# Performance work log

Hardware: AMD Instinct MI355X
Metric: run time of the kernel (lower is better)

The kernel has to match this reference:

```python
import jax, jax.numpy as jnp
import numpy as np

B, K, D, H, ZDIM = 65536, 16, 64, 128, 16

def setup_inputs() -> dict:
    key = jax.random.key(0)
    ks = jax.random.split(key, 20)
    s = 0.05
    inp = {
        'z': jax.random.normal(ks[0], (B, ZDIM), dtype=jnp.float32),
        'y': jax.random.randint(ks[1], (B,), 0, K),
        # backbone: 4 fc blocks (Linear+ReLU)
        'bw0': jax.random.normal(ks[2], (ZDIM, H), dtype=jnp.float32) * s,
        'bb0': jnp.zeros((H,), dtype=jnp.float32),
        'bw1': jax.random.normal(ks[3], (H, H), dtype=jnp.float32) * s,
        'bb1': jnp.zeros((H,), dtype=jnp.float32),
        'bw2': jax.random.normal(ks[4], (H, H), dtype=jnp.float32) * s,
        'bb2': jnp.zeros((H,), dtype=jnp.float32),
        'bw3': jax.random.normal(ks[5], (H, H), dtype=jnp.float32) * s,
        'bb3': jnp.zeros((H,), dtype=jnp.float32),
        # K heads, weights stacked on leading expert axis; layers 0-2 have ReLU, layer 3 does not
        'hw0': jax.random.normal(ks[6], (K, H, H), dtype=jnp.float32) * s,
        'hb0': jnp.zeros((K, H), dtype=jnp.float32),
        'hw1': jax.random.normal(ks[7], (K, H, H), dtype=jnp.float32) * s,
        'hb1': jnp.zeros((K, H), dtype=jnp.float32),
        'hw2': jax.random.normal(ks[8], (K, H, H), dtype=jnp.float32) * s,
        'hb2': jnp.zeros((K, H), dtype=jnp.float32),
        'hw3': jax.random.normal(ks[9], (K, H, D), dtype=jnp.float32) * s,
        'hb3': jnp.zeros((K, D), dtype=jnp.float32),
    }
    return inp

def reference(z, y, bw0, bb0, bw1, bb1, bw2, bb2, bw3, bb3,
              hw0, hb0, hw1, hb1, hw2, hb2, hw3, hb3):
    h = jax.nn.relu(z @ bw0 + bb0)
    h = jax.nn.relu(h @ bw1 + bb1)
    h = jax.nn.relu(h @ bw2 + bb2)
    h = jax.nn.relu(h @ bw3 + bb3)          # [B, H]
    # all K expert heads (faithful to original: compute all, then gather)
    a = jax.nn.relu(jnp.einsum('bi,kij->bkj', h, hw0) + hb0)  # [B, K, H]
    a = jax.nn.relu(jnp.einsum('bki,kij->bkj', a, hw1) + hb1)
    a = jax.nn.relu(jnp.einsum('bki,kij->bkj', a, hw2) + hb2)
    a = jnp.einsum('bki,kij->bkj', a, hw3) + hb3              # [B, K, D], no ReLU
    # select the y-th head per sample
    out = jnp.take_along_axis(a, y[:, None, None], axis=1)[:, 0, :]  # [B, D]
    return out
```

## Files before the change

kernel.cpp:

```cpp
#include <hip/hip_runtime.h>
#include <hip/hip_bf16.h>
#include <stdint.h>


typedef _Float16 f16;
typedef __attribute__((ext_vector_type(4)))  _Float16 f16x4;
typedef __attribute__((ext_vector_type(8)))  _Float16 f16x8;
typedef __attribute__((ext_vector_type(16))) float    f32x16;
typedef uint32_t u32;

#define MFMA(a, b, c) __builtin_amdgcn_mfma_f32_32x32x16_f16((a), (b), (c), 0, 0, 0)

constexpr int Bc = 65536;
constexpr int Kc = 16;
constexpr int Hc = 128;
constexpr int Dc = 64;

constexpr int CAP  = 4608;
constexpr int BPE  = CAP / 64;
constexpr int NBLK = Kc * BPE;

constexpr float INV_LOSCALE = 1.0f / 1024.0f;

constexpr int BBW_F16 = 2048 + 3 * 16384;
constexpr int HWE_F16 = 3 * 16384 + 8192;

constexpr int PREP_BLKS = 52 + Kc * 56;

__device__ __forceinline__ f32x16 zero16() {
    f32x16 z;
#pragma unroll
    for (int i = 0; i < 16; ++i) z[i] = 0.0f;
    return z;
}

__device__ __forceinline__ int actOff(int s, int u) {
    return s * 128 + ((u ^ (s & 15)) << 3);
}

template<bool RELU>
__device__ __forceinline__ void epi_store(
    const f32x16& aH0, const f32x16& aL0,
    const f32x16& aH1, const f32x16& aL1,
    const float* biasLds, f16* aOut, int wid, int l31, int bh)
{
#pragma unroll
    for (int rg = 0; rg < 4; ++rg) {
        const float4 bv = *(const float4*)(biasLds + 32 * wid + 8 * rg + 4 * bh);
        const float bb[4] = {bv.x, bv.y, bv.z, bv.w};
#pragma unroll
        for (int mt = 0; mt < 2; ++mt) {
            const f32x16& aH = mt ? aH1 : aH0;
            const f32x16& aL = mt ? aL1 : aL0;
            f16x4 h4;
#pragma unroll
            for (int j = 0; j < 4; ++j) {
                float v = fmaf(aL[4 * rg + j], INV_LOSCALE, aH[4 * rg + j]) + bb[j];
                if (RELU) v = fmaxf(v, 0.0f);
                h4[j] = (f16)v;
            }
            const int s = 32 * mt + l31;
            *(f16x4*)(aOut + actOff(s, 4 * wid + rg) + 4 * bh) = h4;
        }
    }
}

__device__ __forceinline__ void layer4(
    const f16* __restrict__ Wh, const f16* __restrict__ Wl,
    const float* biasLds, const f16* aIn, f16* aOut,
    int wid, int lane, int l31, int bh)
{
    const f16* ph = Wh + wid * 4096 + lane * 8;
    const f16* pl = Wl + wid * 4096 + lane * 8;

    f32x16 aH0 = zero16(), aH1 = zero16(), aL0 = zero16(), aL1 = zero16();
#pragma unroll
    for (int ks = 0; ks < 8; ++ks) {
        const f16x8 whi = *(const f16x8*)(ph + ks * 512);
        const f16x8 wlo = *(const f16x8*)(pl + ks * 512);
        const f16x8 a0 = *(const f16x8*)(aIn + actOff(l31,      2 * ks + bh));
        const f16x8 a1 = *(const f16x8*)(aIn + actOff(32 + l31, 2 * ks + bh));
        aH0 = MFMA(whi, a0, aH0);
        aH1 = MFMA(whi, a1, aH1);
        aL0 = MFMA(wlo, a0, aL0);
        aL1 = MFMA(wlo, a1, aL1);
    }
    epi_store<true>(aH0, aL0, aH1, aL1, biasLds, aOut, wid, l31, bh);
}

__global__ __launch_bounds__(256, 3) void fused_mlp(
    const float* __restrict__ z,
    const int* __restrict__ idxb, const int* __restrict__ cursor,
    const f16* __restrict__ bbH, const f16* __restrict__ bbL,
    const float* __restrict__ bb0, const float* __restrict__ bb1,
    const float* __restrict__ bb2, const float* __restrict__ bb3,
    const f16* __restrict__ hH, const f16* __restrict__ hL,
    const float* __restrict__ hb0, const float* __restrict__ hb1,
    const float* __restrict__ hb2, const float* __restrict__ hb3,
    float* __restrict__ out)
{
    __shared__ __attribute__((aligned(16))) f16 A[64 * 128];
    __shared__ __attribute__((aligned(16))) f16 B[64 * 128];
    __shared__ __attribute__((aligned(16))) float BIAS[960];
    __shared__ int sidx[64];

    const int blk = blockIdx.x;
    const int e = blk / BPE;
    const int local0 = (blk % BPE) * 64;
    const int cnt = min(cursor[e * 16], CAP);
    const int nvalid = cnt - local0;
    if (nvalid <= 0) return;

    const int tid = threadIdx.x;
    const int wid = tid >> 6, lane = tid & 63;
    const int l31 = lane & 31, bh = lane >> 5;

#pragma unroll
    for (int r = 0; r < 4; ++r) {
        const int i = r * 256 + tid;
        if (i < 960) {
            float v;
            if      (i < 128) v = bb0[i];
            else if (i < 256) v = bb1[i - 128];
            else if (i < 384) v = bb2[i - 256];
            else if (i < 512) v = bb3[i - 384];
            else if (i < 640) v = hb0[e * Hc + i - 512];
            else if (i < 768) v = hb1[e * Hc + i - 640];
            else if (i < 896) v = hb2[e * Hc + i - 768];
            else              v = hb3[e * Dc + i - 896];
            BIAS[i] = v;
        }
    }
    if (tid < 64) sidx[tid] = (tid < nvalid) ? idxb[e * CAP + local0 + tid] : -1;
    __syncthreads();

    {
        const int m = tid >> 2, q = tid & 3;
        const int b = sidx[m];
        f16x4 t;
        if (b >= 0) {
            const float4 v = *(const float4*)(z + (size_t)b * 16 + q * 4);
            t[0] = (f16)v.x; t[1] = (f16)v.y; t[2] = (f16)v.z; t[3] = (f16)v.w;
        } else {
            t[0] = t[1] = t[2] = t[3] = (f16)0.0f;
        }
        *(f16x4*)(A + actOff(m, q >> 1) + (q & 1) * 4) = t;
    }
    __syncthreads();

    {
        const f16x8 w0h = *(const f16x8*)(bbH + wid * 512 + lane * 8);
        const f16x8 w0l = *(const f16x8*)(bbL + wid * 512 + lane * 8);
        const f16x8 a0 = *(const f16x8*)(A + actOff(l31,      bh));
        const f16x8 a1 = *(const f16x8*)(A + actOff(32 + l31, bh));
        f32x16 aH0 = zero16(), aH1 = zero16(), aL0 = zero16(), aL1 = zero16();
        aH0 = MFMA(w0h, a0, aH0);
        aH1 = MFMA(w0h, a1, aH1);
        aL0 = MFMA(w0l, a0, aL0);
        aL1 = MFMA(w0l, a1, aL1);
        epi_store<true>(aH0, aL0, aH1, aL1, BIAS, B, wid, l31, bh);
    }
    __syncthreads();

    layer4(bbH + 2048,  bbL + 2048,  BIAS + 128, B, A, wid, lane, l31, bh);
    __syncthreads();
    layer4(bbH + 18432, bbL + 18432, BIAS + 256, A, B, wid, lane, l31, bh);
    __syncthreads();
    layer4(bbH + 34816, bbL + 34816, BIAS + 384, B, A, wid, lane, l31, bh);
    __syncthreads();

    const size_t we = (size_t)e * HWE_F16;
    layer4(hH + we,         hL + we,         BIAS + 512, A, B, wid, lane, l31, bh);
    __syncthreads();
    layer4(hH + we + 16384, hL + we + 16384, BIAS + 640, B, A, wid, lane, l31, bh);
    __syncthreads();
    layer4(hH + we + 32768, hL + we + 32768, BIAS + 768, A, B, wid, lane, l31, bh);
    __syncthreads();

    if (wid < 2) {
        const f16* ph = hH + we + 49152 + wid * 4096 + lane * 8;
        const f16* pl = hL + we + 49152 + wid * 4096 + lane * 8;
        f32x16 aH0 = zero16(), aH1 = zero16(), aL0 = zero16(), aL1 = zero16();
#pragma unroll
        for (int ks = 0; ks < 8; ++ks) {
            const f16x8 whi = *(const f16x8*)(ph + ks * 512);
            const f16x8 wlo = *(const f16x8*)(pl + ks * 512);
            const f16x8 a0 = *(const f16x8*)(B + actOff(l31,      2 * ks + bh));
            const f16x8 a1 = *(const f16x8*)(B + actOff(32 + l31, 2 * ks + bh));
            aH0 = MFMA(whi, a0, aH0);
            aH1 = MFMA(whi, a1, aH1);
            aL0 = MFMA(wlo, a0, aL0);
            aL1 = MFMA(wlo, a1, aL1);
        }
#pragma unroll
        for (int mt = 0; mt < 2; ++mt) {
            const int b = sidx[32 * mt + l31];
            if (b < 0) continue;
            const f32x16& aH = mt ? aH1 : aH0;
            const f32x16& aL = mt ? aL1 : aL0;
#pragma unroll
            for (int rg = 0; rg < 4; ++rg) {
                const int nb = 32 * wid + 8 * rg + 4 * bh;
                const float4 bv = *(const float4*)(BIAS + 896 + nb);
                float4 v;
                v.x = fmaf(aL[4 * rg + 0], INV_LOSCALE, aH[4 * rg + 0]) + bv.x;
                v.y = fmaf(aL[4 * rg + 1], INV_LOSCALE, aH[4 * rg + 1]) + bv.y;
                v.z = fmaf(aL[4 * rg + 2], INV_LOSCALE, aH[4 * rg + 2]) + bv.z;
                v.w = fmaf(aL[4 * rg + 3], INV_LOSCALE, aH[4 * rg + 3]) + bv.w;
                *(float4*)(out + (size_t)b * Dc + nb) = v;
            }
        }
    }
}

__global__ void prep_scatter(
    const float* __restrict__ bw0, const float* __restrict__ bw1,
    const float* __restrict__ bw2, const float* __restrict__ bw3,
    const float* __restrict__ hw0, const float* __restrict__ hw1,
    const float* __restrict__ hw2, const float* __restrict__ hw3,
    f16* __restrict__ bbH, f16* __restrict__ bbL,
    f16* __restrict__ hH,  f16* __restrict__ hL,
    const int* __restrict__ y, int* __restrict__ idxb, int* __restrict__ cursor)
{
    __shared__ float T[32][33];
    __shared__ int lc[Kc];
    __shared__ int lbase[Kc];
    const int id = blockIdx.x;
    const int tx = threadIdx.x;

    if (id >= PREP_BLKS) {
        if (tx < Kc) lc[tx] = 0;
        __syncthreads();
        const int b = (id - PREP_BLKS) * 256 + tx;
        const int e = y[b];
        const int r = atomicAdd(&lc[e], 1);
        __syncthreads();
        if (tx < Kc) lbase[tx] = atomicAdd(&cursor[tx * 16], lc[tx]);
        __syncthreads();
        const int slot = lbase[e] + r;
        if (slot < CAP) idxb[e * CAP + slot] = b;
        return;
    }

    const float* src; f16 *dh, *dl;
    int K, N, k0, n0;
    bool big;

    if (id < 52) {
        if (id < 4) {
            src = bw0; dh = bbH; dl = bbL;
            K = 16; N = 128; k0 = 0; n0 = id * 32; big = false;
        } else {
            const int t = id - 4;
            const int l = t / 16, tile = t % 16;
            const float* bws[3] = {bw1, bw2, bw3};
            src = bws[l];
            dh = bbH + 2048 + l * 16384;
            dl = bbL + 2048 + l * 16384;
            K = 128; N = 128; big = true;
            k0 = (tile >> 2) * 32; n0 = (tile & 3) * 32;
        }
    } else {
        const int t = id - 52;
        const int e = t / 56, r = t % 56;
        if (r < 48) {
            const int l = r / 16, tile = r % 16;
            const float* hws[3] = {hw0, hw1, hw2};
            src = hws[l] + (size_t)e * 16384;
            dh = hH + (size_t)e * HWE_F16 + l * 16384;
            dl = hL + (size_t)e * HWE_F16 + l * 16384;
            K = 128; N = 128; big = true;
            k0 = (tile >> 2) * 32; n0 = (tile & 3) * 32;
        } else {
            const int r2 = r - 48;
            src = hw3 + (size_t)e * 8192;
            dh = hH + (size_t)e * HWE_F16 + 49152;
            dl = hL + (size_t)e * HWE_F16 + 49152;
            K = 128; N = 64; big = true;
            k0 = (r2 >> 1) * 32; n0 = (r2 & 1) * 32;
        }
    }

    const int c = tx & 31, g = tx >> 5;
#pragma unroll
    for (int i = 0; i < 4; ++i) {
        const int row = g * 4 + i;
        if (k0 + row < K)
            T[c][row] = src[(size_t)(k0 + row) * N + n0 + c];
    }
    __syncthreads();
#pragma unroll
    for (int i = 0; i < 4; ++i) {
        const int n = n0 + g * 4 + i;
        const int k = k0 + c;
        if (k < K) {
            const float v = T[g * 4 + i][c];
            const f16 hi = (f16)v;
            const f16 lo = (f16)((v - (float)hi) * 1024.0f);
            size_t didx;
            if (big)
                didx = (size_t)(n >> 5) * 4096 + (size_t)(k >> 4) * 512
                     + ((k >> 3) & 1) * 256 + (n & 31) * 8 + (k & 7);
            else
                didx = (size_t)(n >> 5) * 512 + (size_t)(k >> 3) * 256
                     + (n & 31) * 8 + (k & 7);
            dh[didx] = hi;
            dl[didx] = lo;
        }
    }
}

extern "C" void kernel_launch(void* const* d_in, const int* in_sizes, int n_in,
                              void* d_out, int out_size, void* d_ws, size_t ws_size,
                              hipStream_t stream)
{
    const float* z   = (const float*)d_in[0];
    const int*   y   = (const int*)d_in[1];
    const float* bw0 = (const float*)d_in[2];
    const float* bb0 = (const float*)d_in[3];
    const float* bw1 = (const float*)d_in[4];
    const float* bb1 = (const float*)d_in[5];
    const float* bw2 = (const float*)d_in[6];
    const float* bb2 = (const float*)d_in[7];
    const float* bw3 = (const float*)d_in[8];
    const float* bb3 = (const float*)d_in[9];
    const float* hw0 = (const float*)d_in[10];
    const float* hb0 = (const float*)d_in[11];
    const float* hw1 = (const float*)d_in[12];
    const float* hb1 = (const float*)d_in[13];
    const float* hw2 = (const float*)d_in[14];
    const float* hb2 = (const float*)d_in[15];
    const float* hw3 = (const float*)d_in[16];
    const float* hb3 = (const float*)d_in[17];
    float* out = (float*)d_out;

    char* p = (char*)d_ws;
    f16* bbH = (f16*)p;  p += (size_t)BBW_F16 * 2;
    f16* bbL = (f16*)p;  p += (size_t)BBW_F16 * 2;
    f16* hH  = (f16*)p;  p += (size_t)Kc * HWE_F16 * 2;
    f16* hL  = (f16*)p;  p += (size_t)Kc * HWE_F16 * 2;
    int* idxb = (int*)p; p += (size_t)Kc * CAP * 4;
    int* cursor = (int*)p;

    hipMemsetAsync(cursor, 0, 256 * sizeof(int), stream);

    prep_scatter<<<PREP_BLKS + Bc / 256, 256, 0, stream>>>(
        bw0, bw1, bw2, bw3, hw0, hw1, hw2, hw3,
        bbH, bbL, hH, hL, y, idxb, cursor);

    fused_mlp<<<NBLK, 256, 0, stream>>>(
        z, idxb, cursor, bbH, bbL, bb0, bb1, bb2, bb3,
        hH, hL, hb0, hb1, hb2, hb3, out);
}
```

Measured before the change: 151.1 us.

## Drop LDS bias staging, remap blocks per XCD, raise occupancy target

Removes the shared-memory bias and index staging, along with its extra barrier. Each wave now loads its bias values and sample indices straight from global memory into registers. Block IDs are remapped so that consecutive blocks of one expert land on the same XCD, which should improve L2 reuse of that expert's weights. The launch bound rises from 3 to 5 blocks per CU to raise occupancy, at the risk of register pressure or spills.

New measurement: 203.3 us. 34.5% more time.

```diff
diff --git a/kernel.cpp b/kernel.cpp
--- a/kernel.cpp
+++ b/kernel.cpp
@@ -19,6 +19,8 @@
 constexpr int CAP  = 4608;
 constexpr int BPE  = CAP / 64;
 constexpr int NBLK = Kc * BPE;
+constexpr int NXCD = 8;
+constexpr int CHUNK = NBLK / NXCD;
 
 constexpr float INV_LOSCALE = 1.0f / 1024.0f;
 
@@ -42,12 +44,11 @@
 __device__ __forceinline__ void epi_store(
     const f32x16& aH0, const f32x16& aL0,
     const f32x16& aH1, const f32x16& aL1,
-    const float* biasLds, f16* aOut, int wid, int l31, int bh)
+    const float4* bv, f16* aOut, int wid, int l31, int bh)
 {
 #pragma unroll
     for (int rg = 0; rg < 4; ++rg) {
-        const float4 bv = *(const float4*)(biasLds + 32 * wid + 8 * rg + 4 * bh);
-        const float bb[4] = {bv.x, bv.y, bv.z, bv.w};
+        const float bb[4] = {bv[rg].x, bv[rg].y, bv[rg].z, bv[rg].w};
 #pragma unroll
         for (int mt = 0; mt < 2; ++mt) {
             const f32x16& aH = mt ? aH1 : aH0;
@@ -67,9 +68,14 @@
 
 __device__ __forceinline__ void layer4(
     const f16* __restrict__ Wh, const f16* __restrict__ Wl,
-    const float* biasLds, const f16* aIn, f16* aOut,
+    const float* __restrict__ biasG, const f16* aIn, f16* aOut,
     int wid, int lane, int l31, int bh)
 {
+    float4 bv[4];
+#pragma unroll
+    for (int rg = 0; rg < 4; ++rg)
+        bv[rg] = *(const float4*)(biasG + 32 * wid + 8 * rg + 4 * bh);
+
     const f16* ph = Wh + wid * 4096 + lane * 8;
     const f16* pl = Wl + wid * 4096 + lane * 8;
 
@@ -85,10 +91,10 @@
         aL0 = MFMA(wlo, a0, aL0);
         aL1 = MFMA(wlo, a1, aL1);
     }
-    epi_store<true>(aH0, aL0, aH1, aL1, biasLds, aOut, wid, l31, bh);
-}
-
-__global__ __launch_bounds__(256, 3) void fused_mlp(
+    epi_store<true>(aH0, aL0, aH1, aL1, bv, aOut, wid, l31, bh);
+}
+
+__global__ __launch_bounds__(256, 5) void fused_mlp(
     const float* __restrict__ z,
     const int* __restrict__ idxb, const int* __restrict__ cursor,
     const f16* __restrict__ bbH, const f16* __restrict__ bbL,
@@ -101,10 +107,8 @@
 {
     __shared__ __attribute__((aligned(16))) f16 A[64 * 128];
     __shared__ __attribute__((aligned(16))) f16 B[64 * 128];
-    __shared__ __attribute__((aligned(16))) float BIAS[960];
-    __shared__ int sidx[64];
-
-    const int blk = blockIdx.x;
+
+    const int blk = (blockIdx.x % NXCD) * CHUNK + blockIdx.x / NXCD;
     const int e = blk / BPE;
     const int local0 = (blk % BPE) * 64;
     const int cnt = min(cursor[e * 16], CAP);
@@ -115,30 +119,11 @@
     const int wid = tid >> 6, lane = tid & 63;
     const int l31 = lane & 31, bh = lane >> 5;
 
-#pragma unroll
-    for (int r = 0; r < 4; ++r) {
-        const int i = r * 256 + tid;
-        if (i < 960) {
-            float v;
-            if      (i < 128) v = bb0[i];
-            else if (i < 256) v = bb1[i - 128];
-            else if (i < 384) v = bb2[i - 256];
-            else if (i < 512) v = bb3[i - 384];
-            else if (i < 640) v = hb0[e * Hc + i - 512];
-            else if (i < 768) v = hb1[e * Hc + i - 640];
-            else if (i < 896) v = hb2[e * Hc + i - 768];
-            else              v = hb3[e * Dc + i - 896];
-            BIAS[i] = v;
-        }
-    }
-    if (tid < 64) sidx[tid] = (tid < nvalid) ? idxb[e * CAP + local0 + tid] : -1;
-    __syncthreads();
-
     {
         const int m = tid >> 2, q = tid & 3;
-        const int b = sidx[m];
         f16x4 t;
-        if (b >= 0) {
+        if (m < nvalid) {
+            const int b = idxb[e * CAP + local0 + m];
             const float4 v = *(const float4*)(z + (size_t)b * 16 + q * 4);
             t[0] = (f16)v.x; t[1] = (f16)v.y; t[2] = (f16)v.z; t[3] = (f16)v.w;
         } else {
@@ -149,6 +134,10 @@
     __syncthreads();
 
     {
+        float4 bv[4];
+#pragma unroll
+        for (int rg = 0; rg < 4; ++rg)
+            bv[rg] = *(const float4*)(bb0 + 32 * wid + 8 * rg + 4 * bh);
         const f16x8 w0h = *(const f16x8*)(bbH + wid * 512 + lane * 8);
         const f16x8 w0l = *(const f16x8*)(bbL + wid * 512 + lane * 8);
         const f16x8 a0 = *(const f16x8*)(A + actOff(l31,      bh));
@@ -158,26 +147,34 @@
         aH1 = MFMA(w0h, a1, aH1);
         aL0 = MFMA(w0l, a0, aL0);
         aL1 = MFMA(w0l, a1, aL1);
-        epi_store<true>(aH0, aL0, aH1, aL1, BIAS, B, wid, l31, bh);
-    }
-    __syncthreads();
-
-    layer4(bbH + 2048,  bbL + 2048,  BIAS + 128, B, A, wid, lane, l31, bh);
-    __syncthreads();
-    layer4(bbH + 18432, bbL + 18432, BIAS + 256, A, B, wid, lane, l31, bh);
-    __syncthreads();
-    layer4(bbH + 34816, bbL + 34816, BIAS + 384, B, A, wid, lane, l31, bh);
+        epi_store<true>(aH0, aL0, aH1, aL1, bv, B, wid, l31, bh);
+    }
+    __syncthreads();
+
+    layer4(bbH + 2048,  bbL + 2048,  bb1, B, A, wid, lane, l31, bh);
+    __syncthreads();
+    layer4(bbH + 18432, bbL + 18432, bb2, A, B, wid, lane, l31, bh);
+    __syncthreads();
+    layer4(bbH + 34816, bbL + 34816, bb3, B, A, wid, lane, l31, bh);
     __syncthreads();
 
     const size_t we = (size_t)e * HWE_F16;
-    layer4(hH + we,         hL + we,         BIAS + 512, A, B, wid, lane, l31, bh);
-    __syncthreads();
-    layer4(hH + we + 16384, hL + we + 16384, BIAS + 640, B, A, wid, lane, l31, bh);
-    __syncthreads();
-    layer4(hH + we + 32768, hL + we + 32768, BIAS + 768, A, B, wid, lane, l31, bh);
+    layer4(hH + we,         hL + we,         hb0 + e * Hc, A, B, wid, lane, l31, bh);
+    __syncthreads();
+    layer4(hH + we + 16384, hL + we + 16384, hb1 + e * Hc, B, A, wid, lane, l31, bh);
+    __syncthreads();
+    layer4(hH + we + 32768, hL + we + 32768, hb2 + e * Hc, A, B, wid, lane, l31, bh);
     __syncthreads();
 
     if (wid < 2) {
+        int b0 = -1, b1 = -1;
+        if (l31 < nvalid)      b0 = idxb[e * CAP + local0 + l31];
+        if (32 + l31 < nvalid) b1 = idxb[e * CAP + local0 + 32 + l31];
+        float4 bvf[4];
+#pragma unroll
+        for (int rg = 0; rg < 4; ++rg)
+            bvf[rg] = *(const float4*)(hb3 + e * Dc + 32 * wid + 8 * rg + 4 * bh);
+
         const f16* ph = hH + we + 49152 + wid * 4096 + lane * 8;
         const f16* pl = hL + we + 49152 + wid * 4096 + lane * 8;
         f32x16 aH0 = zero16(), aH1 = zero16(), aL0 = zero16(), aL1 = zero16();
@@ -194,19 +191,18 @@
         }
 #pragma unroll
         for (int mt = 0; mt < 2; ++mt) {
-            const int b = sidx[32 * mt + l31];
+            const int b = mt ? b1 : b0;
             if (b < 0) continue;
             const f32x16& aH = mt ? aH1 : aH0;
             const f32x16& aL = mt ? aL1 : aL0;
 #pragma unroll
             for (int rg = 0; rg < 4; ++rg) {
                 const int nb = 32 * wid + 8 * rg + 4 * bh;
-                const float4 bv = *(const float4*)(BIAS + 896 + nb);
                 float4 v;
-                v.x = fmaf(aL[4 * rg + 0], INV_LOSCALE, aH[4 * rg + 0]) + bv.x;
-                v.y = fmaf(aL[4 * rg + 1], INV_LOSCALE, aH[4 * rg + 1]) + bv.y;
-                v.z = fmaf(aL[4 * rg + 2], INV_LOSCALE, aH[4 * rg + 2]) + bv.z;
-                v.w = fmaf(aL[4 * rg + 3], INV_LOSCALE, aH[4 * rg + 3]) + bv.w;
+                v.x = fmaf(aL[4 * rg + 0], INV_LOSCALE, aH[4 * rg + 0]) + bvf[rg].x;
+                v.y = fmaf(aL[4 * rg + 1], INV_LOSCALE, aH[4 * rg + 1]) + bvf[rg].y;
+                v.z = fmaf(aL[4 * rg + 2], INV_LOSCALE, aH[4 * rg + 2]) + bvf[rg].z;
+                v.w = fmaf(aL[4 * rg + 3], INV_LOSCALE, aH[4 * rg + 3]) + bvf[rg].w;
                 *(float4*)(out + (size_t)b * Dc + nb) = v;
             }
         }
```
